# Performance work log

Hardware: AMD Instinct MI355X
Metric: run time of the kernel (lower is better)

## Reference

```python
import jax, jax.numpy as jnp
import numpy as np

B, T, N, C, H = 8, 96, 1024, 64, 64  # batch, in_len, nodes, hidden_dim, MLP hidden
NUM_TYPES, EMB = 3, 8
GROUPS = 4


def setup_inputs() -> dict:
    key = jax.random.key(0)
    ks = jax.random.split(key, 16)
    s = 0.05
    return {
        "x": jax.random.normal(ks[0], (B, T, 1, N), jnp.float32),
        "adj": jax.random.uniform(ks[1], (N, N), jnp.float32) / N,  # row-normalized-ish
        "node_type": jax.random.randint(ks[2], (N,), 0, NUM_TYPES),
        # input_projection: Conv1d(1, C, 1) -> per-channel scale + bias
        "w_in": jax.random.normal(ks[3], (C,), jnp.float32) * np.sqrt(2.0),
        "b_in": jnp.zeros((C,), jnp.float32),
        # GCN params
        "weights_pool": jax.random.normal(ks[4], (EMB, C, C), jnp.float32) * np.sqrt(2.0 / (EMB + C)),
        "node_emb": jax.random.normal(ks[5], (NUM_TYPES, EMB), jnp.float32) * s,
        # GroupNorm(4, C)
        "gn_w": jnp.ones((C,), jnp.float32),
        "gn_b": jnp.zeros((C,), jnp.float32),
        # ResBlock temporal MLP: Linear(T,H) then Linear(H,T)
        "w1": jax.random.normal(ks[6], (H, T), jnp.float32) * np.sqrt(1.0 / T),
        "b1": jnp.zeros((H,), jnp.float32),
        "w2": jax.random.normal(ks[7], (T, H), jnp.float32) * np.sqrt(1.0 / H),
        "b2": jnp.zeros((T,), jnp.float32),
        # out_projection: Conv1d(C, 1, 1)
        "w_out": jax.random.normal(ks[8], (C,), jnp.float32) * np.sqrt(2.0 / C),
        "b_out": jnp.zeros((), jnp.float32),
    }


def reference(x, adj, node_type, w_in, b_in, weights_pool, node_emb,
              gn_w, gn_b, w1, b1, w2, b2, w_out, b_out):
    Bx, Tx, _, Nx = x.shape
    BT = Bx * Tx
    # input_projection: Conv1d(1->C, k=1) on (BT, 1, N)
    h = x.reshape(BT, Nx)                                   # channel dim is 1
    h = h[:, None, :] * w_in[None, :, None] + b_in[None, :, None]   # (BT, C, N)
    x_in = h
    # --- GCN with adaptive per-node weights ---
    feats = jnp.swapaxes(h, 1, 2)                            # (BT, N, C)
    nt_emb = node_emb[node_type]                             # gather -> (N, 8)
    node_w = jnp.einsum('nd,dio->nio', nt_emb, weights_pool) # (N, C, C)
    feats = jnp.einsum('nm,bmi->bni', adj, feats)            # adj @ feats
    feats = jnp.einsum('bni,nio->bno', feats, node_w)        # per-node matmul
    h = jnp.swapaxes(feats, 1, 2) + x_in                     # (BT, C, N)
    # --- GroupNorm(4, C), eps=1e-5 ---
    g = h.reshape(BT, GROUPS, C // GROUPS, Nx)
    mu = g.mean(axis=(2, 3), keepdims=True)
    var = g.var(axis=(2, 3), keepdims=True)
    g = (g - mu) / jnp.sqrt(var + 1e-5)
    h = g.reshape(BT, C, Nx) * gn_w[None, :, None] + gn_b[None, :, None]
    # --- temporal mixer: (b t) c n -> (b n) t c ---
    h = h.reshape(Bx, Tx, C, Nx).transpose(0, 3, 1, 2).reshape(Bx * Nx, Tx, C)
    ht = jnp.swapaxes(h, 1, 2)                               # (BN, C, T)
    t = jax.nn.relu(ht @ w1.T + b1) @ w2.T + b2              # (BN, C, T)
    h = h + jnp.swapaxes(t, 1, 2)                            # (BN, T, C)
    # --- silu + out_projection: Conv1d(C->1, k=1) over (BN, C, T) ---
    y = jax.nn.silu(jnp.swapaxes(h, 1, 2))                   # (BN, C, T)
    y = jnp.einsum('bct,c->bt', y, w_out) + b_out            # (BN, T)
    y = y.reshape(Bx, Nx, Tx).transpose(0, 2, 1)[:, :, None, :]  # (B, T, 1, N)
    return y
```

## Files before the change

### kernel.cpp

```cpp
#include <hip/hip_runtime.h>
#include <hip/hip_bf16.h>
#include <math.h>

#define B_   8
#define T_   96
#define N_   1024
#define C_   64
#define H_   64
#define BT_  768
#define EMB_ 8

typedef __attribute__((ext_vector_type(8))) short short8v;
typedef __attribute__((ext_vector_type(4))) float f32x4;

__device__ __forceinline__ ushort f2bf(float f) {
    unsigned int u = __float_as_uint(f);
    unsigned int r = (u + 0x7fffu + ((u >> 16) & 1u)) >> 16;
    return (ushort)r;
}
__device__ __forceinline__ float bf2f(ushort h) {
    return __uint_as_float(((unsigned int)h) << 16);
}

__global__ __launch_bounds__(256) void k_setup(const float* __restrict__ wpool,
                                               const float* __restrict__ w_in,
                                               const float* __restrict__ b_in,
                                               const float* __restrict__ w1,
                                               const float* __restrict__ w2,
                                               const float* __restrict__ x,
                                               float* __restrict__ wp1,
                                               float* __restrict__ wpb,
                                               ushort* __restrict__ wfrag1,
                                               ushort* __restrict__ wfrag2,
                                               float* __restrict__ xT) {
    int bid = blockIdx.x;
    int tid = threadIdx.x;
    if (bid == 0) {
        for (int e = tid; e < EMB_ * C_; e += 256) {
            int d = e >> 6, c = e & 63;
            float s1 = 0.f, s2 = 0.f;
            for (int i = 0; i < C_; ++i) {
                float w = wpool[(d * C_ + i) * C_ + c];
                s1 += w_in[i] * w;
                s2 += b_in[i] * w;
            }
            wp1[e] = s1;
            wpb[e] = s2;
        }
    } else if (bid == 1) {
        for (int e = tid; e < 6144; e += 256) {
            int j = e & 7, lane = (e >> 3) & 63, frag = e >> 9;
            int mt = frag / 3, k0 = frag - 3 * mt;
            int h = 16 * mt + (lane & 15);
            int t = 32 * k0 + 8 * (lane >> 4) + j;
            wfrag1[e] = f2bf(w1[h * T_ + t]);
        }
    } else if (bid == 2) {
        for (int e = tid; e < 6144; e += 256) {
            int j = e & 7, lane = (e >> 3) & 63, frag = e >> 9;
            int mt2 = frag >> 1, ks = frag & 1;
            int t = 16 * mt2 + (lane & 15);
            int h = 32 * ks + 8 * (lane >> 4) + j;
            wfrag2[e] = f2bf(w2[t * H_ + h]);
        }
    } else {
        __shared__ float tile[64][65];
        int tnum = bid - 3;
        int ti = tnum >> 4;
        int tj = tnum & 15;
#pragma unroll
        for (int k = 0; k < 16; ++k) {
            int idx = tid + 256 * k;
            int r = idx >> 6, cq = idx & 63;
            tile[r][cq] = x[(ti * 64 + r) * N_ + tj * 64 + cq];
        }
        __syncthreads();
#pragma unroll
        for (int k = 0; k < 16; ++k) {
            int idx = tid + 256 * k;
            int r = idx >> 6, cq = idx & 63;
            xT[(tj * 64 + r) * BT_ + ti * 64 + cq] = tile[cq][r];
        }
    }
}

__global__ __launch_bounds__(256) void k_tab(const float* __restrict__ wp1,
                                             const float* __restrict__ wpb,
                                             const float* __restrict__ emb,
                                             const float* __restrict__ w_in,
                                             const float* __restrict__ b_in,
                                             float* __restrict__ WT,
                                             float* __restrict__ BTb,
                                             float* __restrict__ TAB,
                                             float* __restrict__ GG) {
    int tid = threadIdx.x;
    int wave = tid >> 6, lane = tid & 63;
    int lq = lane & 15, g = lane >> 4;
    if (wave < 3) {
        int ty = wave, c = lane;
        float w = 0.f, bb = 0.f;
#pragma unroll
        for (int d = 0; d < EMB_; ++d) {
            float ev = emb[ty * EMB_ + d];
            w += ev * wp1[d * C_ + c];
            bb += ev * wpb[d * C_ + c];
        }
        WT[ty * C_ + c] = w;
        BTb[ty * C_ + c] = bb;
        float wi = w_in[c], bi = b_in[c];
        float vals[9] = {w, bb, w * w, bb * bb, w * wi, w * bi, wi * bb, bb * bi, w * bb};
#pragma unroll
        for (int q = 0; q < 9; ++q) {
            vals[q] += __shfl_xor(vals[q], 1);
            vals[q] += __shfl_xor(vals[q], 2);
            vals[q] += __shfl_xor(vals[q], 4);
            vals[q] += __shfl_xor(vals[q], 8);
        }
        if (lq == 0) {
#pragma unroll
            for (int q = 0; q < 9; ++q) TAB[(ty * 4 + g) * 9 + q] = vals[q];
        }
    } else {
        int c = lane;
        float wi = w_in[c], bi = b_in[c];
        float v5[5] = {wi, bi, wi * wi, bi * bi, wi * bi};
#pragma unroll
        for (int q = 0; q < 5; ++q) {
            v5[q] += __shfl_xor(v5[q], 1);
            v5[q] += __shfl_xor(v5[q], 2);
            v5[q] += __shfl_xor(v5[q], 4);
            v5[q] += __shfl_xor(v5[q], 8);
        }
        if (lq == 0) {
#pragma unroll
            for (int q = 0; q < 5; ++q) GG[g * 5 + q] = v5[q];
        }
    }
}

__global__ __launch_bounds__(256, 4) void k_ax(const float* __restrict__ x,
                                               const float* __restrict__ adj,
                                               float* __restrict__ axo,
                                               float* __restrict__ axT,
                                               float* __restrict__ rs) {
    __shared__ ushort Xs[32 * 64];
    __shared__ ushort As[32 * 64];
    const int tid = threadIdx.x;
    const int wave = tid >> 6, lane = tid & 63;
    const int lq = lane & 15, g4 = lane >> 4;
    const int n0 = blockIdx.x * 32, m0 = blockIdx.y * 32;
    const int mi = wave >> 1, ni = wave & 1;
    const int sr = tid >> 3, sq = tid & 7;
    const int sqx = sq ^ (sr & 7);
    const int ra = 16 * mi + lq, rb = 16 * ni + lq;

    f32x4 acc = {0.f, 0.f, 0.f, 0.f};
    float rsacc = 0.f;

    for (int k0 = 0; k0 < N_; k0 += 64) {
        __syncthreads();
        {
            const float* px = x + (m0 + sr) * N_ + k0 + sq * 8;
            float4 xa = *(const float4*)px;
            float4 xb = *(const float4*)(px + 4);
            union { short8v v; __hip_bfloat162 h[4]; } o;
            o.h[0] = __float22bfloat162_rn(make_float2(xa.x, xa.y));
            o.h[1] = __float22bfloat162_rn(make_float2(xa.z, xa.w));
            o.h[2] = __float22bfloat162_rn(make_float2(xb.x, xb.y));
            o.h[3] = __float22bfloat162_rn(make_float2(xb.z, xb.w));
            *(short8v*)&Xs[sr * 64 + sqx * 8] = o.v;

            const float* pa = adj + (n0 + sr) * N_ + k0 + sq * 8;
            float4 aa = *(const float4*)pa;
            float4 ab = *(const float4*)(pa + 4);
            if (m0 == 0)
                rsacc += aa.x + aa.y + aa.z + aa.w + ab.x + ab.y + ab.z + ab.w;
            o.h[0] = __float22bfloat162_rn(make_float2(aa.x, aa.y));
            o.h[1] = __float22bfloat162_rn(make_float2(aa.z, aa.w));
            o.h[2] = __float22bfloat162_rn(make_float2(ab.x, ab.y));
            o.h[3] = __float22bfloat162_rn(make_float2(ab.z, ab.w));
            *(short8v*)&As[sr * 64 + sqx * 8] = o.v;
        }
        __syncthreads();
#pragma unroll
        for (int ks = 0; ks < 2; ++ks) {
            short8v a = *(const short8v*)&Xs[ra * 64 + ((4 * ks + g4) ^ (ra & 7)) * 8];
            short8v bb = *(const short8v*)&As[rb * 64 + ((4 * ks + g4) ^ (rb & 7)) * 8];
            acc = __builtin_amdgcn_mfma_f32_16x16x32_bf16(a, bb, acc, 0, 0, 0);
        }
    }
    if (m0 == 0) {
        rsacc += __shfl_xor(rsacc, 1);
        rsacc += __shfl_xor(rsacc, 2);
        rsacc += __shfl_xor(rsacc, 4);
        if (sq == 0) rs[n0 + sr] = rsacc;
    }
#pragma unroll
    for (int r = 0; r < 4; ++r)
        axo[(m0 + 16 * mi + 4 * g4 + r) * N_ + n0 + 16 * ni + lq] = acc[r];
    float4 tv = make_float4(acc[0], acc[1], acc[2], acc[3]);
    *(float4*)&axT[(n0 + 16 * ni + lq) * BT_ + m0 + 16 * mi + 4 * g4] = tv;
}

__global__ __launch_bounds__(256) void k_gn(const float* __restrict__ x,
                                            const float* __restrict__ ax,
                                            const float* __restrict__ rs,
                                            const int* __restrict__ ntype,
                                            const float* __restrict__ TAB,
                                            const float* __restrict__ GG,
                                            float* __restrict__ muT,
                                            float* __restrict__ rgT) {
    int bt = blockIdx.x;
    int tid = threadIdx.x;
    const float* axr = ax + bt * N_;
    const float* xr = x + bt * N_;
    float S[23];
#pragma unroll
    for (int q = 0; q < 23; ++q) S[q] = 0.f;
#pragma unroll
    for (int i = 0; i < 4; ++i) {
        int n = tid + 256 * i;
        float a = axr[n], xv = xr[n], r = rs[n];
        int ty = ntype[n];
        float e0 = (ty == 0) ? 1.f : 0.f;
        float e1 = (ty == 1) ? 1.f : 0.f;
        float e2 = (ty == 2) ? 1.f : 0.f;
        float a2 = a * a, axp = a * xv, ar = a * r, xrr = xv * r, r2 = r * r;
        S[0] += e0 * a;   S[1] += e1 * a;   S[2] += e2 * a;
        S[3] += e0 * r;   S[4] += e1 * r;   S[5] += e2 * r;
        S[6] += e0 * a2;  S[7] += e1 * a2;  S[8] += e2 * a2;
        S[9] += e0 * r2;  S[10] += e1 * r2; S[11] += e2 * r2;
        S[12] += e0 * axp; S[13] += e1 * axp; S[14] += e2 * axp;
        S[15] += e0 * ar; S[16] += e1 * ar; S[17] += e2 * ar;
        S[18] += e0 * xrr; S[19] += e1 * xrr; S[20] += e2 * xrr;
        S[21] += xv;      S[22] += xv * xv;
    }
#pragma unroll
    for (int q = 0; q < 23; ++q) {
#pragma unroll
        for (int off = 32; off; off >>= 1) S[q] += __shfl_down(S[q], off);
    }
    __shared__ float wred[4][23];
    __shared__ float tot[23];
    int wave = tid >> 6, lane = tid & 63;
    if (lane == 0) {
#pragma unroll
        for (int q = 0; q < 23; ++q) wred[wave][q] = S[q];
    }
    __syncthreads();
    if (tid < 23) tot[tid] = wred[0][tid] + wred[1][tid] + wred[2][tid] + wred[3][tid];
    __syncthreads();
    if (tid < 4) {
        int g = tid;
        float M = 0.f, Q = 0.f;
#pragma unroll
        for (int ty = 0; ty < 3; ++ty) {
            const float* tb = TAB + (ty * 4 + g) * 9;
            float A1v = tot[0 + ty], R1v = tot[3 + ty], A2v = tot[6 + ty];
            float R2v = tot[9 + ty], AXv = tot[12 + ty], ARv = tot[15 + ty];
            float XRv = tot[18 + ty];
            M += tb[0] * A1v + tb[1] * R1v;
            Q += tb[2] * A2v + tb[3] * R2v +
                 2.f * (tb[4] * AXv + tb[5] * A1v + tb[6] * XRv + tb[7] * R1v + tb[8] * ARv);
        }
        float Sx = tot[21], Sx2 = tot[22];
        const float* gg = GG + g * 5;
        M += gg[0] * Sx + 1024.f * gg[1];
        Q += gg[2] * Sx2 + 2.f * gg[4] * Sx + 1024.f * gg[3];
        const float inv = 1.f / 16384.f;
        float m = M * inv;
        float v = Q * inv - m * m;
        int b = bt / T_, t = bt - b * T_;
        muT[(b * 4 + g) * T_ + t] = m;
        rgT[(b * 4 + g) * T_ + t] = rsqrtf(v + 1e-5f);
    }
}

__global__ __launch_bounds__(256, 4) void k_main(const float* __restrict__ xT,
                                                 const float* __restrict__ axT,
                                                 const float* __restrict__ rs,
                                                 const int* __restrict__ ntype,
                                                 const float* __restrict__ WT,
                                                 const float* __restrict__ BTb,
                                                 const float* __restrict__ muT,
                                                 const float* __restrict__ rgT,
                                                 const float* __restrict__ w_in,
                                                 const float* __restrict__ b_in,
                                                 const float* __restrict__ gn_w,
                                                 const float* __restrict__ gn_b,
                                                 const ushort* __restrict__ wfrag1,
                                                 const ushort* __restrict__ wfrag2,
                                                 const float* __restrict__ b1,
                                                 const float* __restrict__ b2,
                                                 const float* __restrict__ w_out,
                                                 const float* __restrict__ b_out,
                                                 float* __restrict__ out) {
    __shared__ ushort Hs[64 * 104];
    __shared__ ushort Hd[64 * 104];
    __shared__ float axs[4][96], xs[4][96];
    __shared__ float musT[4 * 100], rgsT[4 * 100];
    __shared__ float redp[4][96][4];

    const int tid = threadIdx.x;
    const int n0 = blockIdx.x * 4;
    const int b = blockIdx.y;
    const int wm = tid >> 6;
    const int lane = tid & 63;
    const int lq = lane & 15;
    const int g4 = lane >> 4;

    short8v w1f[4][3];
#pragma unroll
    for (int mt = 0; mt < 4; ++mt)
#pragma unroll
        for (int k0 = 0; k0 < 3; ++k0)
            w1f[mt][k0] = *(const short8v*)(wfrag1 + (((mt * 3 + k0) << 6) + lane) * 8);

    for (int j = tid; j < 384; j += 256) {
        int nn = j / 96, t = j - nn * 96;
        axs[nn][t] = axT[(n0 + nn) * BT_ + b * T_ + t];
        xs[nn][t] = xT[(n0 + nn) * BT_ + b * T_ + t];
    }
    for (int j = tid; j < 384; j += 256) {
        int g = j / 96, t = j - 96 * g;
        musT[g * 100 + t] = muT[b * 384 + j];
        rgsT[g * 100 + t] = rgT[b * 384 + j];
    }

    const int c = 16 * wm + lq;
    const float wic = w_in[c], bic = b_in[c];
    const float gwc = gn_w[c], gbc = gn_b[c];
    const float wlcA[3] = {WT[c], WT[64 + c], WT[128 + c]};
    const float blcA[3] = {BTb[c], BTb[64 + c], BTb[128 + c]};
    __syncthreads();

    const ushort* wf2p = wfrag2;
    const float* b1p = b1;
    const float* b2p = b2;
    const float* wop = w_out;

#pragma unroll 1
    for (int nn = 0; nn < 4; ++nn) {
        asm volatile("" : "+s"(wf2p), "+s"(b1p), "+s"(b2p), "+s"(wop));
        const int n = n0 + nn;
        const int ty = ntype[n];
        const float wlc = (ty == 0) ? wlcA[0] : (ty == 1) ? wlcA[1] : wlcA[2];
        const float blc = (ty == 0) ? blcA[0] : (ty == 1) ? blcA[1] : blcA[2];
        const float base = rs[n] * blc + bic;

        f32x4 acc1[4] = {{0.f, 0.f, 0.f, 0.f}, {0.f, 0.f, 0.f, 0.f},
                         {0.f, 0.f, 0.f, 0.f}, {0.f, 0.f, 0.f, 0.f}};
#pragma unroll
        for (int k0 = 0; k0 < 3; ++k0) {
            int t8 = 32 * k0 + 8 * g4;
            float4 a0 = *(const float4*)&axs[nn][t8];
            float4 a1 = *(const float4*)&axs[nn][t8 + 4];
            float4 x0 = *(const float4*)&xs[nn][t8];
            float4 x1 = *(const float4*)&xs[nn][t8 + 4];
            float4 m0 = *(const float4*)&musT[wm * 100 + t8];
            float4 m1 = *(const float4*)&musT[wm * 100 + t8 + 4];
            float4 r0 = *(const float4*)&rgsT[wm * 100 + t8];
            float4 r1 = *(const float4*)&rgsT[wm * 100 + t8 + 4];
            float vv[8];
            vv[0] = ((a0.x * wlc + x0.x * wic + base) - m0.x) * (r0.x * gwc) + gbc;
            vv[1] = ((a0.y * wlc + x0.y * wic + base) - m0.y) * (r0.y * gwc) + gbc;
            vv[2] = ((a0.z * wlc + x0.z * wic + base) - m0.z) * (r0.z * gwc) + gbc;
            vv[3] = ((a0.w * wlc + x0.w * wic + base) - m0.w) * (r0.w * gwc) + gbc;
            vv[4] = ((a1.x * wlc + x1.x * wic + base) - m1.x) * (r1.x * gwc) + gbc;
            vv[5] = ((a1.y * wlc + x1.y * wic + base) - m1.y) * (r1.y * gwc) + gbc;
            vv[6] = ((a1.z * wlc + x1.z * wic + base) - m1.z) * (r1.z * gwc) + gbc;
            vv[7] = ((a1.w * wlc + x1.w * wic + base) - m1.w) * (r1.w * gwc) + gbc;
            union { short8v v; __hip_bfloat162 h2[4]; } o;
            o.h2[0] = __float22bfloat162_rn(make_float2(vv[0], vv[1]));
            o.h2[1] = __float22bfloat162_rn(make_float2(vv[2], vv[3]));
            o.h2[2] = __float22bfloat162_rn(make_float2(vv[4], vv[5]));
            o.h2[3] = __float22bfloat162_rn(make_float2(vv[6], vv[7]));
            *(short8v*)&Hs[c * 104 + t8] = o.v;
#pragma unroll
            for (int mt = 0; mt < 4; ++mt)
                acc1[mt] = __builtin_amdgcn_mfma_f32_16x16x32_bf16(w1f[mt][k0], o.v, acc1[mt], 0, 0, 0);
        }

#pragma unroll
        for (int mt = 0; mt < 4; ++mt) {
            float4 b1v = *(const float4*)(b1p + 16 * mt + 4 * g4);
            __hip_bfloat162 p0 = __float22bfloat162_rn(make_float2(
                fmaxf(acc1[mt][0] + b1v.x, 0.f), fmaxf(acc1[mt][1] + b1v.y, 0.f)));
            __hip_bfloat162 p1 = __float22bfloat162_rn(make_float2(
                fmaxf(acc1[mt][2] + b1v.z, 0.f), fmaxf(acc1[mt][3] + b1v.w, 0.f)));
            union { uint2 u; __hip_bfloat162 h2[2]; } w;
            w.h2[0] = p0; w.h2[1] = p1;
            *(uint2*)&Hd[c * 104 + 16 * mt + 4 * g4] = w.u;
        }

        f32x4 acc2[6] = {{0.f, 0.f, 0.f, 0.f}, {0.f, 0.f, 0.f, 0.f},
                         {0.f, 0.f, 0.f, 0.f}, {0.f, 0.f, 0.f, 0.f},
                         {0.f, 0.f, 0.f, 0.f}, {0.f, 0.f, 0.f, 0.f}};
#pragma unroll
        for (int ks = 0; ks < 2; ++ks) {
            short8v af = *(const short8v*)&Hd[c * 104 + 32 * ks + 8 * g4];
#pragma unroll
            for (int mt2 = 0; mt2 < 6; ++mt2) {
                short8v bf = *(const short8v*)(wf2p + (((mt2 * 2 + ks) << 6) + lane) * 8);
                acc2[mt2] = __builtin_amdgcn_mfma_f32_16x16x32_bf16(af, bf, acc2[mt2], 0, 0, 0);
            }
        }

        float4 wo4 = *(const float4*)(wop + 16 * wm + 4 * g4);
#pragma unroll
        for (int mt2 = 0; mt2 < 6; ++mt2) {
            int tv = 16 * mt2 + lq;
            float bz = b2p[tv];
            float pm = 0.f;
#pragma unroll
            for (int r = 0; r < 4; ++r) {
                float res = bf2f(Hs[(16 * wm + 4 * g4 + r) * 104 + tv]);
                float z = res + acc2[mt2][r] + bz;
                float sg = __builtin_amdgcn_rcpf(1.f + __expf(-z));
                pm += z * sg * wo4[r];
            }
            pm += __shfl_xor(pm, 16);
            pm += __shfl_xor(pm, 32);
            if (g4 == 0) redp[nn][tv][wm] = pm;
        }
    }
    __syncthreads();

    if (tid < 96) {
        float bo = b_out[0];
        float4 y;
        float* py = (float*)&y;
#pragma unroll
        for (int nn = 0; nn < 4; ++nn) {
            float4 v = *(const float4*)&redp[nn][tid][0];
            py[nn] = v.x + v.y + v.z + v.w + bo;
        }
        *(float4*)&out[(b * T_ + tid) * N_ + n0] = y;
    }
}

extern "C" void kernel_launch(void* const* d_in, const int* in_sizes, int n_in,
                              void* d_out, int out_size, void* d_ws, size_t ws_size,
                              hipStream_t stream) {
    const float* x     = (const float*)d_in[0];
    const float* adj   = (const float*)d_in[1];
    const int*   ntype = (const int*)d_in[2];
    const float* w_in  = (const float*)d_in[3];
    const float* b_in  = (const float*)d_in[4];
    const float* wpool = (const float*)d_in[5];
    const float* emb   = (const float*)d_in[6];
    const float* gn_w  = (const float*)d_in[7];
    const float* gn_b  = (const float*)d_in[8];
    const float* w1    = (const float*)d_in[9];
    const float* b1    = (const float*)d_in[10];
    const float* w2    = (const float*)d_in[11];
    const float* b2    = (const float*)d_in[12];
    const float* w_out = (const float*)d_in[13];
    const float* b_out = (const float*)d_in[14];
    float* out = (float*)d_out;
    float* ws = (float*)d_ws;

    float* wp1  = ws;
    float* wpb  = ws + 512;
    float* rsv  = ws + 1024;
    float* WT   = ws + 2048;
    float* BTb  = ws + 2240;
    float* TAB  = ws + 2432;
    float* GG   = ws + 2540;
    float* muT  = ws + 2560;
    float* rgT  = ws + 5632;
    ushort* wfrag1 = (ushort*)(ws + 8704);
    ushort* wfrag2 = (ushort*)(ws + 11776);
    float* axb  = ws + 14848;
    float* axTb = ws + 14848 + 786432;
    float* xTb  = ws + 14848 + 2 * 786432;

    k_setup<<<dim3(195), dim3(256), 0, stream>>>(wpool, w_in, b_in, w1, w2, x,
                                                 wp1, wpb, wfrag1, wfrag2, xTb);
    k_tab<<<dim3(1), dim3(256), 0, stream>>>(wp1, wpb, emb, w_in, b_in,
                                             WT, BTb, TAB, GG);
    k_ax<<<dim3(32, 24), dim3(256), 0, stream>>>(x, adj, axb, axTb, rsv);
    k_gn<<<dim3(768), dim3(256), 0, stream>>>(x, axb, rsv, ntype, TAB, GG, muT, rgT);
    k_main<<<dim3(256, 8), dim3(256), 0, stream>>>(xTb, axTb, rsv, ntype, WT, BTb,
                                                   muT, rgT, w_in, b_in, gn_w, gn_b,
                                                   wfrag1, wfrag2, b1, b2,
                                                   w_out, b_out, out);
}
```

Baseline: 81.93 us.

## Merge setup kernels, cut k_main registers and LDS, use atomic output

Folds the k_tab kernel into the last block of k_setup through shared memory, removing one launch. In k_main, w1 fragments are loaded from global memory per use instead of held in registers. GroupNorm constants are prefolded, biases go into the accumulator init, and launch bounds rise to 5 blocks per SM. The shared-memory final reduction is replaced with per-wave atomicAdd into an output zeroed by a memset. This adds a memset launch and atomic traffic, and makes the summation order nondeterministic.

```diff
diff --git a/kernel.cpp b/kernel.cpp
--- a/kernel.cpp
+++ b/kernel.cpp
@@ -25,29 +25,20 @@
 __global__ __launch_bounds__(256) void k_setup(const float* __restrict__ wpool,
                                                const float* __restrict__ w_in,
                                                const float* __restrict__ b_in,
+                                               const float* __restrict__ emb,
                                                const float* __restrict__ w1,
                                                const float* __restrict__ w2,
                                                const float* __restrict__ x,
-                                               float* __restrict__ wp1,
-                                               float* __restrict__ wpb,
                                                ushort* __restrict__ wfrag1,
                                                ushort* __restrict__ wfrag2,
-                                               float* __restrict__ xT) {
+                                               float* __restrict__ xT,
+                                               float* __restrict__ WT,
+                                               float* __restrict__ BTb,
+                                               float* __restrict__ TAB,
+                                               float* __restrict__ GG) {
     int bid = blockIdx.x;
     int tid = threadIdx.x;
     if (bid == 0) {
-        for (int e = tid; e < EMB_ * C_; e += 256) {
-            int d = e >> 6, c = e & 63;
-            float s1 = 0.f, s2 = 0.f;
-            for (int i = 0; i < C_; ++i) {
-                float w = wpool[(d * C_ + i) * C_ + c];
-                s1 += w_in[i] * w;
-                s2 += b_in[i] * w;
-            }
-            wp1[e] = s1;
-            wpb[e] = s2;
-        }
-    } else if (bid == 1) {
         for (int e = tid; e < 6144; e += 256) {
             int j = e & 7, lane = (e >> 3) & 63, frag = e >> 9;
             int mt = frag / 3, k0 = frag - 3 * mt;
@@ -55,7 +46,7 @@
             int t = 32 * k0 + 8 * (lane >> 4) + j;
             wfrag1[e] = f2bf(w1[h * T_ + t]);
         }
-    } else if (bid == 2) {
+    } else if (bid == 1) {
         for (int e = tid; e < 6144; e += 256) {
             int j = e & 7, lane = (e >> 3) & 63, frag = e >> 9;
             int mt2 = frag >> 1, ks = frag & 1;
@@ -63,9 +54,9 @@
             int h = 32 * ks + 8 * (lane >> 4) + j;
             wfrag2[e] = f2bf(w2[t * H_ + h]);
         }
-    } else {
+    } else if (bid < 194) {
         __shared__ float tile[64][65];
-        int tnum = bid - 3;
+        int tnum = bid - 2;
         int ti = tnum >> 4;
         int tj = tnum & 15;
 #pragma unroll
@@ -81,59 +72,61 @@
             int r = idx >> 6, cq = idx & 63;
             xT[(tj * 64 + r) * BT_ + ti * 64 + cq] = tile[cq][r];
         }
-    }
-}
-
-__global__ __launch_bounds__(256) void k_tab(const float* __restrict__ wp1,
-                                             const float* __restrict__ wpb,
-                                             const float* __restrict__ emb,
-                                             const float* __restrict__ w_in,
-                                             const float* __restrict__ b_in,
-                                             float* __restrict__ WT,
-                                             float* __restrict__ BTb,
-                                             float* __restrict__ TAB,
-                                             float* __restrict__ GG) {
-    int tid = threadIdx.x;
-    int wave = tid >> 6, lane = tid & 63;
-    int lq = lane & 15, g = lane >> 4;
-    if (wave < 3) {
-        int ty = wave, c = lane;
-        float w = 0.f, bb = 0.f;
-#pragma unroll
-        for (int d = 0; d < EMB_; ++d) {
-            float ev = emb[ty * EMB_ + d];
-            w += ev * wp1[d * C_ + c];
-            bb += ev * wpb[d * C_ + c];
-        }
-        WT[ty * C_ + c] = w;
-        BTb[ty * C_ + c] = bb;
-        float wi = w_in[c], bi = b_in[c];
-        float vals[9] = {w, bb, w * w, bb * bb, w * wi, w * bi, wi * bb, bb * bi, w * bb};
-#pragma unroll
-        for (int q = 0; q < 9; ++q) {
-            vals[q] += __shfl_xor(vals[q], 1);
-            vals[q] += __shfl_xor(vals[q], 2);
-            vals[q] += __shfl_xor(vals[q], 4);
-            vals[q] += __shfl_xor(vals[q], 8);
-        }
-        if (lq == 0) {
-#pragma unroll
-            for (int q = 0; q < 9; ++q) TAB[(ty * 4 + g) * 9 + q] = vals[q];
-        }
     } else {
-        int c = lane;
-        float wi = w_in[c], bi = b_in[c];
-        float v5[5] = {wi, bi, wi * wi, bi * bi, wi * bi};
-#pragma unroll
-        for (int q = 0; q < 5; ++q) {
-            v5[q] += __shfl_xor(v5[q], 1);
-            v5[q] += __shfl_xor(v5[q], 2);
-            v5[q] += __shfl_xor(v5[q], 4);
-            v5[q] += __shfl_xor(v5[q], 8);
-        }
-        if (lq == 0) {
-#pragma unroll
-            for (int q = 0; q < 5; ++q) GG[g * 5 + q] = v5[q];
+        __shared__ float wp1s[512], wpbs[512];
+        for (int e = tid; e < 512; e += 256) {
+            int d = e >> 6, cc = e & 63;
+            float s1 = 0.f, s2 = 0.f;
+            for (int i = 0; i < 64; ++i) {
+                float w = wpool[(d * 64 + i) * 64 + cc];
+                s1 += w_in[i] * w;
+                s2 += b_in[i] * w;
+            }
+            wp1s[e] = s1;
+            wpbs[e] = s2;
+        }
+        __syncthreads();
+        int wave = tid >> 6, lane = tid & 63;
+        int lq = lane & 15, g = lane >> 4;
+        if (wave < 3) {
+            int ty = wave, cc = lane;
+            float w = 0.f, bb = 0.f;
+#pragma unroll
+            for (int d = 0; d < EMB_; ++d) {
+                float ev = emb[ty * EMB_ + d];
+                w += ev * wp1s[d * C_ + cc];
+                bb += ev * wpbs[d * C_ + cc];
+            }
+            WT[ty * C_ + cc] = w;
+            BTb[ty * C_ + cc] = bb;
+            float wi = w_in[cc], bi = b_in[cc];
+            float vals[9] = {w, bb, w * w, bb * bb, w * wi, w * bi, wi * bb, bb * bi, w * bb};
+#pragma unroll
+            for (int q = 0; q < 9; ++q) {
+                vals[q] += __shfl_xor(vals[q], 1);
+                vals[q] += __shfl_xor(vals[q], 2);
+                vals[q] += __shfl_xor(vals[q], 4);
+                vals[q] += __shfl_xor(vals[q], 8);
+            }
+            if (lq == 0) {
+#pragma unroll
+                for (int q = 0; q < 9; ++q) TAB[(ty * 4 + g) * 9 + q] = vals[q];
+            }
+        } else {
+            int cc = lane;
+            float wi = w_in[cc], bi = b_in[cc];
+            float v5[5] = {wi, bi, wi * wi, bi * bi, wi * bi};
+#pragma unroll
+            for (int q = 0; q < 5; ++q) {
+                v5[q] += __shfl_xor(v5[q], 1);
+                v5[q] += __shfl_xor(v5[q], 2);
+                v5[q] += __shfl_xor(v5[q], 4);
+                v5[q] += __shfl_xor(v5[q], 8);
+            }
+            if (lq == 0) {
+#pragma unroll
+                for (int q = 0; q < 5; ++q) GG[g * 5 + q] = v5[q];
+            }
         }
     }
 }
@@ -276,7 +269,7 @@
     }
 }
 
-__global__ __launch_bounds__(256, 4) void k_main(const float* __restrict__ xT,
+__global__ __launch_bounds__(256, 5) void k_main(const float* __restrict__ xT,
                                                  const float* __restrict__ axT,
                                                  const float* __restrict__ rs,
                                                  const int* __restrict__ ntype,
@@ -298,8 +291,7 @@
     __shared__ ushort Hs[64 * 104];
     __shared__ ushort Hd[64 * 104];
     __shared__ float axs[4][96], xs[4][96];
-    __shared__ float musT[4 * 100], rgsT[4 * 100];
-    __shared__ float redp[4][96][4];
+    __shared__ float rgS[4][96], mgS[4][96];
 
     const int tid = threadIdx.x;
     const int n0 = blockIdx.x * 4;
@@ -309,13 +301,6 @@
     const int lq = lane & 15;
     const int g4 = lane >> 4;
 
-    short8v w1f[4][3];
-#pragma unroll
-    for (int mt = 0; mt < 4; ++mt)
-#pragma unroll
-        for (int k0 = 0; k0 < 3; ++k0)
-            w1f[mt][k0] = *(const short8v*)(wfrag1 + (((mt * 3 + k0) << 6) + lane) * 8);
-
     for (int j = tid; j < 384; j += 256) {
         int nn = j / 96, t = j - nn * 96;
         axs[nn][t] = axT[(n0 + nn) * BT_ + b * T_ + t];
@@ -323,33 +308,45 @@
     }
     for (int j = tid; j < 384; j += 256) {
         int g = j / 96, t = j - 96 * g;
-        musT[g * 100 + t] = muT[b * 384 + j];
-        rgsT[g * 100 + t] = rgT[b * 384 + j];
+        float rg = rgT[b * 384 + j];
+        rgS[g][t] = rg;
+        mgS[g][t] = -muT[b * 384 + j] * rg;
     }
 
     const int c = 16 * wm + lq;
-    const float wic = w_in[c], bic = b_in[c];
     const float gwc = gn_w[c], gbc = gn_b[c];
-    const float wlcA[3] = {WT[c], WT[64 + c], WT[128 + c]};
-    const float blcA[3] = {BTb[c], BTb[64 + c], BTb[128 + c]};
+    const float wicg = w_in[c] * gwc;
+    const float bicg = b_in[c] * gwc;
+    const float wlcg[3] = {WT[c] * gwc, WT[64 + c] * gwc, WT[128 + c] * gwc};
+    const float blcg[3] = {BTb[c] * gwc, BTb[64 + c] * gwc, BTb[128 + c] * gwc};
+    float b2q[6];
+#pragma unroll
+    for (int mt2 = 0; mt2 < 6; ++mt2) b2q[mt2] = b2[16 * mt2 + lq];
+    const float4 wo4 = *(const float4*)&w_out[16 * wm + 4 * g4];
+    const float bo4 = 0.25f * b_out[0];
     __syncthreads();
 
+    const ushort* wf1p = wfrag1;
     const ushort* wf2p = wfrag2;
     const float* b1p = b1;
-    const float* b2p = b2;
-    const float* wop = w_out;
 
 #pragma unroll 1
     for (int nn = 0; nn < 4; ++nn) {
-        asm volatile("" : "+s"(wf2p), "+s"(b1p), "+s"(b2p), "+s"(wop));
+        asm volatile("" : "+s"(wf1p), "+s"(wf2p), "+s"(b1p));
         const int n = n0 + nn;
         const int ty = ntype[n];
-        const float wlc = (ty == 0) ? wlcA[0] : (ty == 1) ? wlcA[1] : wlcA[2];
-        const float blc = (ty == 0) ? blcA[0] : (ty == 1) ? blcA[1] : blcA[2];
-        const float base = rs[n] * blc + bic;
-
-        f32x4 acc1[4] = {{0.f, 0.f, 0.f, 0.f}, {0.f, 0.f, 0.f, 0.f},
-                         {0.f, 0.f, 0.f, 0.f}, {0.f, 0.f, 0.f, 0.f}};
+        const float wlc = (ty == 0) ? wlcg[0] : (ty == 1) ? wlcg[1] : wlcg[2];
+        const float blc = (ty == 0) ? blcg[0] : (ty == 1) ? blcg[1] : blcg[2];
+        const float base = fmaf(rs[n], blc, bicg);
+
+        f32x4 acc1[4];
+#pragma unroll
+        for (int mt = 0; mt < 4; ++mt) {
+            float4 b1v = *(const float4*)(b1p + 16 * mt + 4 * g4);
+            acc1[mt][0] = b1v.x; acc1[mt][1] = b1v.y;
+            acc1[mt][2] = b1v.z; acc1[mt][3] = b1v.w;
+        }
+
 #pragma unroll
         for (int k0 = 0; k0 < 3; ++k0) {
             int t8 = 32 * k0 + 8 * g4;
@@ -357,19 +354,19 @@
             float4 a1 = *(const float4*)&axs[nn][t8 + 4];
             float4 x0 = *(const float4*)&xs[nn][t8];
             float4 x1 = *(const float4*)&xs[nn][t8 + 4];
-            float4 m0 = *(const float4*)&musT[wm * 100 + t8];
-            float4 m1 = *(const float4*)&musT[wm * 100 + t8 + 4];
-            float4 r0 = *(const float4*)&rgsT[wm * 100 + t8];
-            float4 r1 = *(const float4*)&rgsT[wm * 100 + t8 + 4];
+            float4 r0 = *(const float4*)&rgS[wm][t8];
+            float4 r1 = *(const float4*)&rgS[wm][t8 + 4];
+            float4 m0 = *(const float4*)&mgS[wm][t8];
+            float4 m1 = *(const float4*)&mgS[wm][t8 + 4];
             float vv[8];
-            vv[0] = ((a0.x * wlc + x0.x * wic + base) - m0.x) * (r0.x * gwc) + gbc;
-            vv[1] = ((a0.y * wlc + x0.y * wic + base) - m0.y) * (r0.y * gwc) + gbc;
-            vv[2] = ((a0.z * wlc + x0.z * wic + base) - m0.z) * (r0.z * gwc) + gbc;
-            vv[3] = ((a0.w * wlc + x0.w * wic + base) - m0.w) * (r0.w * gwc) + gbc;
-            vv[4] = ((a1.x * wlc + x1.x * wic + base) - m1.x) * (r1.x * gwc) + gbc;
-            vv[5] = ((a1.y * wlc + x1.y * wic + base) - m1.y) * (r1.y * gwc) + gbc;
-            vv[6] = ((a1.z * wlc + x1.z * wic + base) - m1.z) * (r1.z * gwc) + gbc;
-            vv[7] = ((a1.w * wlc + x1.w * wic + base) - m1.w) * (r1.w * gwc) + gbc;
+            vv[0] = fmaf(fmaf(x0.x, wicg, fmaf(a0.x, wlc, base)), r0.x, fmaf(m0.x, gwc, gbc));
+            vv[1] = fmaf(fmaf(x0.y, wicg, fmaf(a0.y, wlc, base)), r0.y, fmaf(m0.y, gwc, gbc));
+            vv[2] = fmaf(fmaf(x0.z, wicg, fmaf(a0.z, wlc, base)), r0.z, fmaf(m0.z, gwc, gbc));
+            vv[3] = fmaf(fmaf(x0.w, wicg, fmaf(a0.w, wlc, base)), r0.w, fmaf(m0.w, gwc, gbc));
+            vv[4] = fmaf(fmaf(x1.x, wicg, fmaf(a1.x, wlc, base)), r1.x, fmaf(m1.x, gwc, gbc));
+            vv[5] = fmaf(fmaf(x1.y, wicg, fmaf(a1.y, wlc, base)), r1.y, fmaf(m1.y, gwc, gbc));
+            vv[6] = fmaf(fmaf(x1.z, wicg, fmaf(a1.z, wlc, base)), r1.z, fmaf(m1.z, gwc, gbc));
+            vv[7] = fmaf(fmaf(x1.w, wicg, fmaf(a1.w, wlc, base)), r1.w, fmaf(m1.w, gwc, gbc));
             union { short8v v; __hip_bfloat162 h2[4]; } o;
             o.h2[0] = __float22bfloat162_rn(make_float2(vv[0], vv[1]));
             o.h2[1] = __float22bfloat162_rn(make_float2(vv[2], vv[3]));
@@ -377,25 +374,29 @@
             o.h2[3] = __float22bfloat162_rn(make_float2(vv[6], vv[7]));
             *(short8v*)&Hs[c * 104 + t8] = o.v;
 #pragma unroll
-            for (int mt = 0; mt < 4; ++mt)
-                acc1[mt] = __builtin_amdgcn_mfma_f32_16x16x32_bf16(w1f[mt][k0], o.v, acc1[mt], 0, 0, 0);
+            for (int mt = 0; mt < 4; ++mt) {
+                short8v wv = *(const short8v*)(wf1p + (((mt * 3 + k0) << 6) + lane) * 8);
+                acc1[mt] = __builtin_amdgcn_mfma_f32_16x16x32_bf16(wv, o.v, acc1[mt], 0, 0, 0);
+            }
         }
 
 #pragma unroll
         for (int mt = 0; mt < 4; ++mt) {
-            float4 b1v = *(const float4*)(b1p + 16 * mt + 4 * g4);
             __hip_bfloat162 p0 = __float22bfloat162_rn(make_float2(
-                fmaxf(acc1[mt][0] + b1v.x, 0.f), fmaxf(acc1[mt][1] + b1v.y, 0.f)));
+                fmaxf(acc1[mt][0], 0.f), fmaxf(acc1[mt][1], 0.f)));
             __hip_bfloat162 p1 = __float22bfloat162_rn(make_float2(
-                fmaxf(acc1[mt][2] + b1v.z, 0.f), fmaxf(acc1[mt][3] + b1v.w, 0.f)));
+                fmaxf(acc1[mt][2], 0.f), fmaxf(acc1[mt][3], 0.f)));
             union { uint2 u; __hip_bfloat162 h2[2]; } w;
             w.h2[0] = p0; w.h2[1] = p1;
             *(uint2*)&Hd[c * 104 + 16 * mt + 4 * g4] = w.u;
         }
 
-        f32x4 acc2[6] = {{0.f, 0.f, 0.f, 0.f}, {0.f, 0.f, 0.f, 0.f},
-                         {0.f, 0.f, 0.f, 0.f}, {0.f, 0.f, 0.f, 0.f},
-                         {0.f, 0.f, 0.f, 0.f}, {0.f, 0.f, 0.f, 0.f}};
+        f32x4 acc2[6];
+#pragma unroll
+        for (int mt2 = 0; mt2 < 6; ++mt2) {
+            float bv = b2q[mt2];
+            acc2[mt2][0] = bv; acc2[mt2][1] = bv; acc2[mt2][2] = bv; acc2[mt2][3] = bv;
+        }
 #pragma unroll
         for (int ks = 0; ks < 2; ++ks) {
             short8v af = *(const short8v*)&Hd[c * 104 + 32 * ks + 8 * g4];
@@ -406,36 +407,22 @@
             }
         }
 
-        float4 wo4 = *(const float4*)(wop + 16 * wm + 4 * g4);
 #pragma unroll
         for (int mt2 = 0; mt2 < 6; ++mt2) {
             int tv = 16 * mt2 + lq;
-            float bz = b2p[tv];
             float pm = 0.f;
 #pragma unroll
             for (int r = 0; r < 4; ++r) {
                 float res = bf2f(Hs[(16 * wm + 4 * g4 + r) * 104 + tv]);
-                float z = res + acc2[mt2][r] + bz;
+                float z = res + acc2[mt2][r];
                 float sg = __builtin_amdgcn_rcpf(1.f + __expf(-z));
-                pm += z * sg * wo4[r];
+                pm = fmaf(z * sg, wo4[r], pm);
             }
             pm += __shfl_xor(pm, 16);
             pm += __shfl_xor(pm, 32);
-            if (g4 == 0) redp[nn][tv][wm] = pm;
-        }
-    }
-    __syncthreads();
-
-    if (tid < 96) {
-        float bo = b_out[0];
-        float4 y;
-        float* py = (float*)&y;
-#pragma unroll
-        for (int nn = 0; nn < 4; ++nn) {
-            float4 v = *(const float4*)&redp[nn][tid][0];
-            py[nn] = v.x + v.y + v.z + v.w + bo;
-        }
-        *(float4*)&out[(b * T_ + tid) * N_ + n0] = y;
+            if (g4 == 0)
+                atomicAdd(&out[(b * T_ + tv) * N_ + n], pm + bo4);
+        }
     }
 }
 
@@ -460,8 +447,6 @@
     float* out = (float*)d_out;
     float* ws = (float*)d_ws;
 
-    float* wp1  = ws;
-    float* wpb  = ws + 512;
     float* rsv  = ws + 1024;
     float* WT   = ws + 2048;
     float* BTb  = ws + 2240;
@@ -475,10 +460,9 @@
     float* axTb = ws + 14848 + 786432;
     float* xTb  = ws + 14848 + 2 * 786432;
 
-    k_setup<<<dim3(195), dim3(256), 0, stream>>>(wpool, w_in, b_in, w1, w2, x,
-                                                 wp1, wpb, wfrag1, wfrag2, xTb);
-    k_tab<<<dim3(1), dim3(256), 0, stream>>>(wp1, wpb, emb, w_in, b_in,
-                                             WT, BTb, TAB, GG);
+    hipMemsetAsync(out, 0, (size_t)out_size * sizeof(float), stream);
+    k_setup<<<dim3(195), dim3(256), 0, stream>>>(wpool, w_in, b_in, emb, w1, w2, x,
+                                                 wfrag1, wfrag2, xTb, WT, BTb, TAB, GG);
     k_ax<<<dim3(32, 24), dim3(256), 0, stream>>>(x, adj, axb, axTb, rsv);
     k_gn<<<dim3(768), dim3(256), 0, stream>>>(x, axb, rsv, ntype, TAB, GG, muT, rgT);
     k_main<<<dim3(256, 8), dim3(256), 0, stream>>>(xTb, axTb, rsv, ntype, WT, BTb,
```

Result: slower. 206.6 us (+152.2%).
